# Optimization experiments

Hardware: AMD Instinct MI355X
Metric: run time of the kernel (lower is better)

## Reference

```python
import jax, jax.numpy as jnp
import numpy as np

D = 1024
B, S = 4, 2048

def setup_inputs() -> dict:
    key = jax.random.key(0)
    ks = jax.random.split(key, 9)
    scale = 1.0 / np.sqrt(D)
    return {
        "queries": jax.random.normal(ks[0], (B, S, D), dtype=jnp.float32),
        "keys": jax.random.normal(ks[1], (B, S, D), dtype=jnp.float32),
        "values": jax.random.normal(ks[2], (B, S, D), dtype=jnp.float32),
        # torch nn.Linear weights: [out, in], y = x @ W.T + b
        "Wq": jax.random.uniform(ks[3], (D, D), jnp.float32, -scale, scale),
        "bq": jax.random.uniform(ks[4], (D,), jnp.float32, -scale, scale),
        "Wk": jax.random.uniform(ks[5], (D, D), jnp.float32, -scale, scale),
        "bk": jax.random.uniform(ks[6], (D,), jnp.float32, -scale, scale),
        "Wv": jax.random.uniform(ks[7], (D, D), jnp.float32, -scale, scale),
        "bv": jax.random.uniform(ks[8], (D,), jnp.float32, -scale, scale),
    }

def reference(queries, keys, values, Wq, bq, Wk, bk, Wv, bv):
    # Linear projections (torch convention: x @ W.T + b)
    Q = jnp.einsum('bsd,ed->bse', queries, Wq) + bq  # [B,S,D]
    K = jnp.einsum('bsd,ed->bse', keys, Wk) + bk
    V = jnp.einsum('bsd,ed->bse', values, Wv) + bv
    # relu attention: no softmax, no scaling (faithful to source)
    scores = jax.nn.relu(jnp.einsum('bqd,bkd->bqk', Q, K))  # [B,S,S]
    return jnp.einsum('bqk,bkd->bqd', scores, V)
```

## Files before the change

kernel.cpp:

```cpp
#include <hip/hip_runtime.h>
#include <hip/hip_bf16.h>
#include <stdint.h>

typedef __bf16 bf16_t;
typedef __bf16 bf16x8 __attribute__((ext_vector_type(8)));
typedef float  f32x16 __attribute__((ext_vector_type(16)));

__device__ __forceinline__ void async_copy16(const bf16_t* g, bf16_t* l) {
    __builtin_amdgcn_global_load_lds(
        (const __attribute__((address_space(1))) unsigned int*)(uintptr_t)g,
        (__attribute__((address_space(3))) unsigned int*)(uintptr_t)l,
        16, 0, 0);
}

template<int N> __device__ __forceinline__ void vmw() {
    if constexpr (N == 0)      asm volatile("s_waitcnt vmcnt(0)");
    else if constexpr (N == 5) asm volatile("s_waitcnt vmcnt(5)");
    else if constexpr (N == 6) asm volatile("s_waitcnt vmcnt(6)");
}
#define BARR() __builtin_amdgcn_s_barrier()


#define STAGEA(buf, h, kt) do {                                                   \
    _Pragma("unroll") for (int j = 0; j < LA; j++)                                \
        async_copy16(ApM + (long)(h)*(BM/2)*K + (long)(kt)*64 + offA[j],          \
                     (bf16_t*)(lds + (buf)*BUF + (h)*HBYTES + dstA[j]));          \
} while (0)

#define STAGEB(buf, h, kt) do {                                                   \
    _Pragma("unroll") for (int j = 0; j < 2; j++)                                 \
        async_copy16(BpN + (long)(h)*128*K + (long)(kt)*64 + offB[j],             \
                     (bf16_t*)(lds + (buf)*BUF + ABYTES + (h)*16384 + dstB[j]));  \
} while (0)

#define LOADA(buf, hA) do {                                                       \
    _Pragma("unroll") for (int m = 0; m < MT; m++)                                \
    _Pragma("unroll") for (int ks = 0; ks < 4; ks++) {                            \
        const int R = (hA)*(BM/2) + sr*(BM/4) + m*32 + r32;                       \
        af[m][ks] = *(const bf16x8*)(lds + (buf)*BUF + R*128                      \
                                     + (((ks*2 + half) ^ (R & 7)) << 4));         \
    } } while (0)

#define LOADB(buf, hB) do {                                                       \
    _Pragma("unroll") for (int ks = 0; ks < 4; ks++) {                            \
        const int Cc = (hB)*128 + sc*32 + r32;                                    \
        bf[hB][ks] = *(const bf16x8*)(lds + (buf)*BUF + ABYTES + Cc*128           \
                                      + (((ks*2 + half) ^ (Cc & 7)) << 4));       \
    } } while (0)

#define MMA(hA, hB) do {                                                          \
    __builtin_amdgcn_s_setprio(1);                                                \
    _Pragma("unroll") for (int m = 0; m < MT; m++)                                \
    _Pragma("unroll") for (int ks = 0; ks < 4; ks++)                              \
        acc[hA][hB][m] = __builtin_amdgcn_mfma_f32_32x32x16_bf16(                 \
            af[m][ks], bf[hB][ks], acc[hA][hB][m], 0, 0, 0);                      \
    __builtin_amdgcn_s_setprio(0);                                                \
} while (0)

template<int BM, bool OUT_F32, bool RELU, int BIAS_MODE, bool BIAS_SPLIT>
__global__ __launch_bounds__(512, 2)
void gemm256(const bf16_t* __restrict__ A, const bf16_t* __restrict__ B,
             const float* __restrict__ bias0, const float* __restrict__ bias1,
             void* __restrict__ Cp,
             int K, int ldc, long sAb, long sBb, long sCb)
{
    constexpr int MT     = BM / 128;
    constexpr int LA     = BM / 128;
    constexpr int VMN    = 4 + LA;
    constexpr int ABYTES = BM * 128;
    constexpr int HBYTES = ABYTES / 2;
    constexpr int BUF    = ABYTES + 32768;

    __shared__ char lds[2 * BUF];

    const int gx = gridDim.x, gy = gridDim.y;
    const int tot = gx * gy * gridDim.z;
    const int lin = (blockIdx.z * gy + blockIdx.y) * gx + blockIdx.x;
    const int q8  = tot >> 3;
    const int wg  = (lin & 7) * q8 + (lin >> 3);
    const int bz  = wg / (gx * gy);
    const int r2  = wg - bz * gx * gy;
    const int by  = r2 / gx;
    const int bx  = r2 - by * gx;
    const int blockM = by * BM;
    const int blockN = bx * 256;

    const int t    = threadIdx.x;
    const int lane = t & 63;
    const int wave = t >> 6;
    const int sr   = wave >> 2;
    const int sc   = wave & 3;
    const int r32  = lane & 31;
    const int half = lane >> 5;

    const bf16_t* ApM = A + sAb * (long)bz + (long)blockM * K;
    const bf16_t* BpN = B + sBb * (long)bz + (long)blockN * K;

    long offA[LA]; uint32_t dstA[LA];
    #pragma unroll
    for (int j = 0; j < LA; j++) {
        const int c = t + j * 512, r = c >> 3, s = c & 7;
        offA[j] = (long)r * K + ((s ^ (r & 7)) * 8);
        dstA[j] = (uint32_t)c * 16;
    }
    long offB[2]; uint32_t dstB[2];
    #pragma unroll
    for (int j = 0; j < 2; j++) {
        const int c = t + j * 512, r = c >> 3, s = c & 7;
        offB[j] = (long)r * K + ((s ^ (r & 7)) * 8);
        dstB[j] = (uint32_t)c * 16;
    }

    f32x16 acc[2][2][MT] = {};
    bf16x8 af[MT][4];
    bf16x8 bf[2][4];

    const int NT = K >> 6;
    const int NI = NT >> 1;

    STAGEA(0, 0, 0); STAGEB(0, 0, 0); STAGEB(0, 1, 0); STAGEA(0, 1, 0);
    STAGEA(1, 0, 1); STAGEB(1, 0, 1); STAGEB(1, 1, 1);
    vmw<VMN>();
    BARR();

    for (int i = 0; i < NI; ++i) {
        const int  T  = 2 * i;
        const bool nl = (i < NI - 1);

        LOADA(0, 0); LOADB(0, 0);
        STAGEA(1, 1, T + 1);
        if constexpr (MT == 2) asm volatile("s_waitcnt lgkmcnt(8)");
        BARR();
        MMA(0, 0);
        BARR();
        LOADB(0, 1);
        if (nl) STAGEA(0, 0, T + 2);
        BARR();
        MMA(0, 1);
        BARR();
        LOADA(0, 1);
        if (nl) STAGEB(0, 0, T + 2);
        BARR();
        MMA(1, 0);
        BARR();
        if (nl) STAGEB(0, 1, T + 2);
        BARR();
        MMA(1, 1);
        if (nl) vmw<VMN>(); else vmw<0>();
        BARR();
        LOADA(1, 0); LOADB(1, 0);
        if (nl) STAGEA(0, 1, T + 2);
        if constexpr (MT == 2) asm volatile("s_waitcnt lgkmcnt(8)");
        BARR();
        MMA(0, 0);
        BARR();
        LOADB(1, 1);
        if (nl) STAGEA(1, 0, T + 3);
        BARR();
        MMA(0, 1);
        BARR();
        LOADA(1, 1);
        if (nl) STAGEB(1, 0, T + 3);
        BARR();
        MMA(1, 0);
        BARR();
        if (nl) STAGEB(1, 1, T + 3);
        BARR();
        MMA(1, 1);
        if (nl) vmw<VMN>();
        BARR();
    }

    float*  Cf = (float*) Cp + sCb * (long)bz;
    bf16_t* Ch = (bf16_t*)Cp + sCb * (long)bz;
    const float* bias = (BIAS_SPLIT && bz) ? bias1 : bias0;
    #pragma unroll
    for (int hA = 0; hA < 2; hA++)
    #pragma unroll
    for (int hB = 0; hB < 2; hB++)
    #pragma unroll
    for (int m = 0; m < MT; m++) {
        const int gcol = blockN + hB * 128 + sc * 32 + r32;
        float bc = 0.f;
        if (BIAS_MODE == 1) bc = bias[gcol];
        #pragma unroll
        for (int reg = 0; reg < 16; reg++) {
            const int grow = blockM + hA * (BM / 2) + sr * (BM / 4) + m * 32
                           + (reg & 3) + 8 * (reg >> 2) + 4 * half;
            float vv = acc[hA][hB][m][reg];
            if (BIAS_MODE == 1) vv += bc;
            if (BIAS_MODE == 2) vv += bias[grow];
            if (RELU) vv = fmaxf(vv, 0.f);
            if (OUT_F32) Cf[(long)grow * ldc + gcol] = vv;
            else         Ch[(long)grow * ldc + gcol] = (bf16_t)vv;
        }
    }
}

__global__ __launch_bounds__(256)
void cast_all_kernel(const float* __restrict__ q, const float* __restrict__ k,
                     const float* __restrict__ v, const float* __restrict__ Wq,
                     const float* __restrict__ Wk, const float* __restrict__ Wv,
                     bf16_t* __restrict__ ws)
{
    const long BIG = 1048576;
    const long SMALL = 131072;
    long id = (long)blockIdx.x * blockDim.x + threadIdx.x;
    const float* src; bf16_t* dst;
    if (id < 3 * BIG) {
        int s = (int)(id / BIG);
        long off = (id - (long)s * BIG) * 8;
        src = (s == 0 ? q : s == 1 ? k : v) + off;
        dst = ws + (long)s * 8388608 + off;
    } else {
        long id2 = id - 3 * BIG;
        int s = (int)(id2 / SMALL);
        long off = (id2 - (long)s * SMALL) * 8;
        src = (s == 0 ? Wq : s == 1 ? Wk : Wv) + off;
        dst = ws + 25165824L + (long)s * 1048576 + off;
    }
    float4 v0 = ((const float4*)src)[0];
    float4 v1 = ((const float4*)src)[1];
    alignas(16) bf16_t o[8];
    o[0]=(bf16_t)v0.x; o[1]=(bf16_t)v0.y; o[2]=(bf16_t)v0.z; o[3]=(bf16_t)v0.w;
    o[4]=(bf16_t)v1.x; o[5]=(bf16_t)v1.y; o[6]=(bf16_t)v1.z; o[7]=(bf16_t)v1.w;
    *(uint4*)dst = *(const uint4*)o;
}

extern "C" void kernel_launch(void* const* d_in, const int* in_sizes, int n_in,
                              void* d_out, int out_size, void* d_ws, size_t ws_size,
                              hipStream_t stream)
{
    const float* q   = (const float*)d_in[0];
    const float* k   = (const float*)d_in[1];
    const float* v   = (const float*)d_in[2];
    const float* Wq  = (const float*)d_in[3];
    const float* bq  = (const float*)d_in[4];
    const float* Wk  = (const float*)d_in[5];
    const float* bk  = (const float*)d_in[6];
    const float* Wv  = (const float*)d_in[7];
    const float* bv  = (const float*)d_in[8];

    const int S = 2048, D = 1024;

    bf16_t* ws  = (bf16_t*)d_ws;
    bf16_t* qb  = ws;
    bf16_t* vb  = ws + 16777216L;
    bf16_t* Wqb = ws + 25165824L;
    bf16_t* Wvb = ws + 27262976L;
    bf16_t* Qp  = ws + 28311552L;
    bf16_t* VpT = ws + 45088768L;
    bf16_t* Sc  = ws;

    cast_all_kernel<<<dim3(13824), dim3(256), 0, stream>>>(q, k, v, Wq, Wk, Wv, ws);

    dim3 blk(512);

    gemm256<256, false, false, 1, true><<<dim3(4, 32, 2), blk, 0, stream>>>(
        qb, Wqb, bq, bk, Qp, D, D, 8388608L, 1048576L, 8388608L);

    gemm256<128, false, false, 2, false><<<dim3(8, 8, 4), blk, 0, stream>>>(
        Wvb, vb, bv, nullptr, VpT, D, S, 0L, (long)S * D, (long)D * S);

    gemm256<256, false, true, 0, false><<<dim3(8, 8, 4), blk, 0, stream>>>(
        Qp, Qp + 8388608L, nullptr, nullptr, Sc, D, S,
        (long)S * D, (long)S * D, (long)S * S);

    gemm256<128, true, false, 0, false><<<dim3(4, 16, 4), blk, 0, stream>>>(
        Sc, VpT, nullptr, nullptr, d_out, S, D,
        (long)S * S, (long)D * S, (long)S * D);
}
```

Before: 294.9 us.

## Switch GEMM MFMA to 16x16x32 tiles and widen cast kernel per-thread work

The GEMM inner product moves from 32x32x16 to 16x16x32 bf16 MFMA instructions, with the LDS fragment loads and the epilogue index mapping rewritten to match. The explicit lgkmcnt waits are dropped. Separately, the fp32-to-bf16 cast kernel now converts 16 elements per thread in a grid-stride loop and launches a quarter of the blocks. The two changes are unrelated; the MFMA swap alters fragment sizes, register use and LDS access patterns, and it is unclear which instruction shape gives better throughput here.

```diff
diff --git a/kernel.cpp b/kernel.cpp
--- a/kernel.cpp
+++ b/kernel.cpp
@@ -4,7 +4,7 @@
 
 typedef __bf16 bf16_t;
 typedef __bf16 bf16x8 __attribute__((ext_vector_type(8)));
-typedef float  f32x16 __attribute__((ext_vector_type(16)));
+typedef float  f32x4  __attribute__((ext_vector_type(4)));
 
 __device__ __forceinline__ void async_copy16(const bf16_t* g, bf16_t* l) {
     __builtin_amdgcn_global_load_lds(
@@ -34,26 +34,28 @@
 } while (0)
 
 #define LOADA(buf, hA) do {                                                       \
-    _Pragma("unroll") for (int m = 0; m < MT; m++)                                \
-    _Pragma("unroll") for (int ks = 0; ks < 4; ks++) {                            \
-        const int R = (hA)*(BM/2) + sr*(BM/4) + m*32 + r32;                       \
-        af[m][ks] = *(const bf16x8*)(lds + (buf)*BUF + R*128                      \
-                                     + (((ks*2 + half) ^ (R & 7)) << 4));         \
+    _Pragma("unroll") for (int m = 0; m < MF; m++)                                \
+    _Pragma("unroll") for (int ks = 0; ks < 2; ks++) {                            \
+        const int R = (hA)*(BM/2) + sr*(BM/4) + m*16 + l15;                       \
+        afr[m][ks] = *(const bf16x8*)(lds + (buf)*BUF + R*128                     \
+                                      + (((ks*4 + l4) ^ (l15 & 7)) << 4));        \
     } } while (0)
 
 #define LOADB(buf, hB) do {                                                       \
-    _Pragma("unroll") for (int ks = 0; ks < 4; ks++) {                            \
-        const int Cc = (hB)*128 + sc*32 + r32;                                    \
-        bf[hB][ks] = *(const bf16x8*)(lds + (buf)*BUF + ABYTES + Cc*128           \
-                                      + (((ks*2 + half) ^ (Cc & 7)) << 4));       \
+    _Pragma("unroll") for (int n = 0; n < 2; n++)                                 \
+    _Pragma("unroll") for (int ks = 0; ks < 2; ks++) {                            \
+        const int Cc = (hB)*128 + sc*32 + n*16 + l15;                             \
+        bfr[hB][n][ks] = *(const bf16x8*)(lds + (buf)*BUF + ABYTES + Cc*128       \
+                                          + (((ks*4 + l4) ^ (l15 & 7)) << 4));    \
     } } while (0)
 
 #define MMA(hA, hB) do {                                                          \
     __builtin_amdgcn_s_setprio(1);                                                \
-    _Pragma("unroll") for (int m = 0; m < MT; m++)                                \
-    _Pragma("unroll") for (int ks = 0; ks < 4; ks++)                              \
-        acc[hA][hB][m] = __builtin_amdgcn_mfma_f32_32x32x16_bf16(                 \
-            af[m][ks], bf[hB][ks], acc[hA][hB][m], 0, 0, 0);                      \
+    _Pragma("unroll") for (int m = 0; m < MF; m++)                                \
+    _Pragma("unroll") for (int n = 0; n < 2; n++)                                 \
+    _Pragma("unroll") for (int ks = 0; ks < 2; ks++)                              \
+        acc[hA][hB][m][n] = __builtin_amdgcn_mfma_f32_16x16x32_bf16(              \
+            afr[m][ks], bfr[hB][n][ks], acc[hA][hB][m][n], 0, 0, 0);              \
     __builtin_amdgcn_s_setprio(0);                                                \
 } while (0)
 
@@ -64,7 +66,7 @@
              void* __restrict__ Cp,
              int K, int ldc, long sAb, long sBb, long sCb)
 {
-    constexpr int MT     = BM / 128;
+    constexpr int MF     = BM / 64;
     constexpr int LA     = BM / 128;
     constexpr int VMN    = 4 + LA;
     constexpr int ABYTES = BM * 128;
@@ -90,8 +92,8 @@
     const int wave = t >> 6;
     const int sr   = wave >> 2;
     const int sc   = wave & 3;
-    const int r32  = lane & 31;
-    const int half = lane >> 5;
+    const int l15  = lane & 15;
+    const int l4   = lane >> 4;
 
     const bf16_t* ApM = A + sAb * (long)bz + (long)blockM * K;
     const bf16_t* BpN = B + sBb * (long)bz + (long)blockN * K;
@@ -111,9 +113,9 @@
         dstB[j] = (uint32_t)c * 16;
     }
 
-    f32x16 acc[2][2][MT] = {};
-    bf16x8 af[MT][4];
-    bf16x8 bf[2][4];
+    f32x4  acc[2][2][MF][2] = {};
+    bf16x8 afr[MF][2];
+    bf16x8 bfr[2][2][2];
 
     const int NT = K >> 6;
     const int NI = NT >> 1;
@@ -129,7 +131,6 @@
 
         LOADA(0, 0); LOADB(0, 0);
         STAGEA(1, 1, T + 1);
-        if constexpr (MT == 2) asm volatile("s_waitcnt lgkmcnt(8)");
         BARR();
         MMA(0, 0);
         BARR();
@@ -150,7 +151,6 @@
         BARR();
         LOADA(1, 0); LOADB(1, 0);
         if (nl) STAGEA(0, 1, T + 2);
-        if constexpr (MT == 2) asm volatile("s_waitcnt lgkmcnt(8)");
         BARR();
         MMA(0, 0);
         BARR();
@@ -179,15 +179,17 @@
     #pragma unroll
     for (int hB = 0; hB < 2; hB++)
     #pragma unroll
-    for (int m = 0; m < MT; m++) {
-        const int gcol = blockN + hB * 128 + sc * 32 + r32;
+    for (int m = 0; m < MF; m++)
+    #pragma unroll
+    for (int n = 0; n < 2; n++) {
+        const int gcol = blockN + hB * 128 + sc * 32 + n * 16 + l15;
         float bc = 0.f;
         if (BIAS_MODE == 1) bc = bias[gcol];
         #pragma unroll
-        for (int reg = 0; reg < 16; reg++) {
-            const int grow = blockM + hA * (BM / 2) + sr * (BM / 4) + m * 32
-                           + (reg & 3) + 8 * (reg >> 2) + 4 * half;
-            float vv = acc[hA][hB][m][reg];
+        for (int reg = 0; reg < 4; reg++) {
+            const int grow = blockM + hA * (BM / 2) + sr * (BM / 4) + m * 16
+                           + l4 * 4 + reg;
+            float vv = acc[hA][hB][m][n][reg];
             if (BIAS_MODE == 1) vv += bc;
             if (BIAS_MODE == 2) vv += bias[grow];
             if (RELU) vv = fmaxf(vv, 0.f);
@@ -203,28 +205,36 @@
                      const float* __restrict__ Wk, const float* __restrict__ Wv,
                      bf16_t* __restrict__ ws)
 {
-    const long BIG = 1048576;
-    const long SMALL = 131072;
-    long id = (long)blockIdx.x * blockDim.x + threadIdx.x;
-    const float* src; bf16_t* dst;
-    if (id < 3 * BIG) {
-        int s = (int)(id / BIG);
-        long off = (id - (long)s * BIG) * 8;
-        src = (s == 0 ? q : s == 1 ? k : v) + off;
-        dst = ws + (long)s * 8388608 + off;
-    } else {
-        long id2 = id - 3 * BIG;
-        int s = (int)(id2 / SMALL);
-        long off = (id2 - (long)s * SMALL) * 8;
-        src = (s == 0 ? Wq : s == 1 ? Wk : Wv) + off;
-        dst = ws + 25165824L + (long)s * 1048576 + off;
-    }
-    float4 v0 = ((const float4*)src)[0];
-    float4 v1 = ((const float4*)src)[1];
-    alignas(16) bf16_t o[8];
-    o[0]=(bf16_t)v0.x; o[1]=(bf16_t)v0.y; o[2]=(bf16_t)v0.z; o[3]=(bf16_t)v0.w;
-    o[4]=(bf16_t)v1.x; o[5]=(bf16_t)v1.y; o[6]=(bf16_t)v1.z; o[7]=(bf16_t)v1.w;
-    *(uint4*)dst = *(const uint4*)o;
+    const int U_BIG   = 524288;
+    const int U_SMALL = 65536;
+    const int U_TOT   = 3 * U_BIG + 3 * U_SMALL;
+    const int stride  = gridDim.x * blockDim.x;
+    for (int u = blockIdx.x * blockDim.x + threadIdx.x; u < U_TOT; u += stride) {
+        const float* src; bf16_t* dst;
+        if (u < 3 * U_BIG) {
+            const int s = u / U_BIG;
+            const long off = (long)(u - s * U_BIG) * 16;
+            src = (s == 0 ? q : s == 1 ? k : v) + off;
+            dst = ws + (long)s * 8388608 + off;
+        } else {
+            const int u2 = u - 3 * U_BIG;
+            const int s = u2 / U_SMALL;
+            const long off = (long)(u2 - s * U_SMALL) * 16;
+            src = (s == 0 ? Wq : s == 1 ? Wk : Wv) + off;
+            dst = ws + 25165824L + (long)s * 1048576 + off;
+        }
+        float4 a = ((const float4*)src)[0];
+        float4 b = ((const float4*)src)[1];
+        float4 c = ((const float4*)src)[2];
+        float4 d = ((const float4*)src)[3];
+        alignas(16) bf16_t o[16];
+        o[0]=(bf16_t)a.x;  o[1]=(bf16_t)a.y;  o[2]=(bf16_t)a.z;  o[3]=(bf16_t)a.w;
+        o[4]=(bf16_t)b.x;  o[5]=(bf16_t)b.y;  o[6]=(bf16_t)b.z;  o[7]=(bf16_t)b.w;
+        o[8]=(bf16_t)c.x;  o[9]=(bf16_t)c.y;  o[10]=(bf16_t)c.z; o[11]=(bf16_t)c.w;
+        o[12]=(bf16_t)d.x; o[13]=(bf16_t)d.y; o[14]=(bf16_t)d.z; o[15]=(bf16_t)d.w;
+        ((uint4*)dst)[0] = *(const uint4*)&o[0];
+        ((uint4*)dst)[1] = *(const uint4*)&o[8];
+    }
 }
 
 extern "C" void kernel_launch(void* const* d_in, const int* in_sizes, int n_in,
@@ -252,7 +262,7 @@
     bf16_t* VpT = ws + 45088768L;
     bf16_t* Sc  = ws;
 
-    cast_all_kernel<<<dim3(13824), dim3(256), 0, stream>>>(q, k, v, Wq, Wk, Wv, ws);
+    cast_all_kernel<<<dim3(3456), dim3(256), 0, stream>>>(q, k, v, Wq, Wk, Wv, ws);
 
     dim3 blk(512);
 
```

Measured after the change: 285.4 us. -3.2%, faster.
